# Performance work log

Hardware: AMD Instinct MI355X
Metric: run time of the kernel (lower is better)

## Reference

```python
import jax, jax.numpy as jnp
import numpy as np

B, S = 4, 1024          # 4 prefill sequences of length 1024 (cu_seqlens equal-length)
D_MODEL = 2048
N_HEADS = 32
N_KV_HEADS = 8
HEAD_DIM = D_MODEL // N_HEADS          # 64
GROUPS = N_HEADS // N_KV_HEADS         # 4
ROPE_THETA = 10000.0
SCALE = HEAD_DIM ** -0.5


def setup_inputs() -> dict:
    key = jax.random.key(0)
    ks = jax.random.split(key, 6)
    T = B * S
    hidden_states = jax.random.normal(ks[0], (T, D_MODEL), jnp.float32)
    # rotary tables: positions restart per sequence (prefill)
    pos = jnp.tile(jnp.arange(S, dtype=jnp.float32), B)            # [T]
    inv_freq = 1.0 / (ROPE_THETA ** (jnp.arange(0, HEAD_DIM, 2, dtype=jnp.float32) / HEAD_DIM))
    freqs = pos[:, None] * inv_freq[None, :]                        # [T, HEAD_DIM/2]
    cos, sin = jnp.cos(freqs), jnp.sin(freqs)
    std = D_MODEL ** -0.5
    Wq = jax.random.normal(ks[1], (D_MODEL, N_HEADS * HEAD_DIM), jnp.float32) * std
    Wk = jax.random.normal(ks[2], (D_MODEL, N_KV_HEADS * HEAD_DIM), jnp.float32) * std
    Wv = jax.random.normal(ks[3], (D_MODEL, N_KV_HEADS * HEAD_DIM), jnp.float32) * std
    Wo = jax.random.normal(ks[4], (N_HEADS * HEAD_DIM, D_MODEL), jnp.float32) * std
    return {"hidden_states": hidden_states, "cos": cos, "sin": sin,
            "Wq": Wq, "Wk": Wk, "Wv": Wv, "Wo": Wo}


def _rope(x, cos, sin):
    # NeoX-style rotary: x [T, H, D], cos/sin [T, D/2]
    half = x.shape[-1] // 2
    x1, x2 = x[..., :half], x[..., half:]
    c, s = cos[:, None, :], sin[:, None, :]
    return jnp.concatenate([x1 * c - x2 * s, x2 * c + x1 * s], axis=-1)


def reference(hidden_states, cos, sin, Wq, Wk, Wv, Wo):
    T = hidden_states.shape[0]
    q = (hidden_states @ Wq).reshape(T, N_HEADS, HEAD_DIM)
    k = (hidden_states @ Wk).reshape(T, N_KV_HEADS, HEAD_DIM)
    v = (hidden_states @ Wv).reshape(T, N_KV_HEADS, HEAD_DIM)
    q = _rope(q, cos, sin)
    k = _rope(k, cos, sin)
    # equal-length varlen prefill -> [B, S, H, D]
    q = q.reshape(B, S, N_HEADS, HEAD_DIM)
    k = jnp.repeat(k.reshape(B, S, N_KV_HEADS, HEAD_DIM), GROUPS, axis=2)  # GQA expand
    v = jnp.repeat(v.reshape(B, S, N_KV_HEADS, HEAD_DIM), GROUPS, axis=2)
    scores = jnp.einsum("bqhd,bkhd->bhqk", q, k) * SCALE
    causal = jnp.tril(jnp.ones((S, S), dtype=bool))
    scores = jnp.where(causal[None, None], scores, jnp.finfo(scores.dtype).min)
    probs = jax.nn.softmax(scores, axis=-1)
    attn = jnp.einsum("bhqk,bkhd->bqhd", probs, v).reshape(T, N_HEADS * HEAD_DIM)
    return attn @ Wo
```

## Files before the change

kernel.cpp:

```cpp
#include <hip/hip_runtime.h>
#include <type_traits>


typedef __bf16 bf16x8 __attribute__((ext_vector_type(8)));
typedef __bf16 bf16x4 __attribute__((ext_vector_type(4)));
typedef float f32x4 __attribute__((ext_vector_type(4)));
typedef unsigned short u16;
typedef unsigned int u32;

#define DEVI __device__ __forceinline__

DEVI u16 f2bf(float f) {
  u32 u = __builtin_bit_cast(u32, f);
  u += 0x7FFF + ((u >> 16) & 1);
  return (u16)(u >> 16);
}

DEVI void ld16_lds(const void* g, void* l) {
  __builtin_amdgcn_global_load_lds((const __attribute__((address_space(1))) u32*)g,
                                   (__attribute__((address_space(3))) u32*)l, 16, 0, 0);
}

template <int N> DEVI void waitvm() {
  if constexpr (N == 0) asm volatile("s_waitcnt vmcnt(0)" ::: "memory");
  else if constexpr (N == 6) asm volatile("s_waitcnt vmcnt(6)" ::: "memory");
  else if constexpr (N == 7) asm volatile("s_waitcnt vmcnt(7)" ::: "memory");
  else static_assert(N == 0, "unsupported vmcnt");
}
DEVI void lgkm0() {
  asm volatile("s_waitcnt lgkmcnt(0)" ::: "memory");
  __builtin_amdgcn_sched_barrier(0);
}
DEVI void barrier() { __builtin_amdgcn_s_barrier(); }

__global__ __launch_bounds__(256) void convert_f32_bf16(const float* __restrict__ src,
                                                        u16* __restrict__ dst, int n4) {
  int i = blockIdx.x * 256 + threadIdx.x;
  if (i >= n4) return;
  float4 v = ((const float4*)src)[i];
  ushort4 o;
  o.x = f2bf(v.x); o.y = f2bf(v.y); o.z = f2bf(v.z); o.w = f2bf(v.w);
  ((ushort4*)dst)[i] = o;
}

__global__ __launch_bounds__(256) void trans_f32_bf16(const float* __restrict__ src,
                                                      u16* __restrict__ dst, int R, int C,
                                                      float scale) {
  __shared__ float tile[32][33];
  int c0 = blockIdx.x * 32, r0 = blockIdx.y * 32;
  int tx = threadIdx.x & 31, ty = threadIdx.x >> 5;
#pragma unroll
  for (int i = 0; i < 32; i += 8)
    tile[ty + i][tx] = src[(size_t)(r0 + ty + i) * C + (c0 + tx)];
  __syncthreads();
#pragma unroll
  for (int i = 0; i < 32; i += 8)
    dst[(size_t)(c0 + ty + i) * R + (r0 + tx)] = f2bf(tile[tx][ty + i] * scale);
}

template <typename OutT, int BN>
__global__ __launch_bounds__(512, 2) void gemm8(const u16* __restrict__ A,
                                                const u16* __restrict__ BT,
                                                OutT* __restrict__ C, int M, int N, int K) {
  constexpr int WN = BN / 64;
  constexpr int NH0 = (WN + 1) / 2;
  constexpr int NH1 = WN - NH0;
  constexpr int VMW = 4 + WN;
  __shared__ u16 As[2][256 * 64];
  __shared__ u16 Bs[2][BN * 64];
  const int tid = threadIdx.x;
  const int lane = tid & 63, wave = tid >> 6;
  const int quad = lane >> 4, l16 = lane & 15;

  const int nwg = gridDim.x * gridDim.y;
  const int bid = blockIdx.y * gridDim.x + blockIdx.x;
  const int swz = (bid & 7) * (nwg >> 3) + (bid >> 3);
  const int m0 = (swz / gridDim.x) * 256, n0 = (swz % gridDim.x) * BN;
  const int wr = wave >> 2, wc = wave & 3;

  f32x4 acc[8][WN] = {};

  auto stageA = [&](int t, int h) {
    u16* D = &As[t & 1][h * 8192];
    const u16* G = A + (size_t)m0 * K + t * 64;
#pragma unroll
    for (int i = 0; i < 2; ++i) {
      int id = i * 512 + tid;
      int row = h * 128 + (id >> 3), ch = id & 7;
      ld16_lds(G + (size_t)row * K + (ch ^ (row & 7)) * 8, D + id * 8);
    }
  };
  auto stageB = [&](int t, int u) {
    u16* D = &Bs[t & 1][u * 4096];
    const u16* G = BT + (size_t)n0 * K + t * 64;
    int row = u * 64 + (tid >> 3), ch = tid & 7;
    ld16_lds(G + (size_t)row * K + (ch ^ (row & 7)) * 8, D + tid * 8);
  };
  auto stageBall = [&](int t) {
#pragma unroll
    for (int u = 0; u < WN; ++u) stageB(t, u);
  };

  bf16x8 af[4][2], bv0[NH0][2], bv1[NH1][2];
  auto ldA = [&](int msub, int d) {
#pragma unroll
    for (int i = 0; i < 4; ++i)
#pragma unroll
      for (int ks = 0; ks < 2; ++ks) {
        int r = wr * 128 + msub * 64 + i * 16 + l16;
        af[i][ks] = *(const bf16x8*)&As[d][r * 64 + (((ks * 4 + quad) ^ (r & 7)) * 8)];
      }
  };
  auto ldB0 = [&](int d) {
#pragma unroll
    for (int j = 0; j < NH0; ++j)
#pragma unroll
      for (int ks = 0; ks < 2; ++ks) {
        int rb = wc * (16 * WN) + j * 16 + l16;
        bv0[j][ks] = *(const bf16x8*)&Bs[d][rb * 64 + (((ks * 4 + quad) ^ (rb & 7)) * 8)];
      }
  };
  auto ldB1 = [&](int d) {
#pragma unroll
    for (int j = 0; j < NH1; ++j)
#pragma unroll
      for (int ks = 0; ks < 2; ++ks) {
        int rb = wc * (16 * WN) + (NH0 + j) * 16 + l16;
        bv1[j][ks] = *(const bf16x8*)&Bs[d][rb * 64 + (((ks * 4 + quad) ^ (rb & 7)) * 8)];
      }
  };
  auto mm0 = [&](int mo) {
    __builtin_amdgcn_s_setprio(1);
#pragma unroll
    for (int i = 0; i < 4; ++i)
#pragma unroll
      for (int j = 0; j < NH0; ++j)
#pragma unroll
        for (int ks = 0; ks < 2; ++ks)
          acc[mo + i][j] =
              __builtin_amdgcn_mfma_f32_16x16x32_bf16(af[i][ks], bv0[j][ks], acc[mo + i][j], 0, 0, 0);
    __builtin_amdgcn_s_setprio(0);
  };
  auto mm1 = [&](int mo) {
    __builtin_amdgcn_s_setprio(1);
#pragma unroll
    for (int i = 0; i < 4; ++i)
#pragma unroll
      for (int j = 0; j < NH1; ++j)
#pragma unroll
        for (int ks = 0; ks < 2; ++ks)
          acc[mo + i][NH0 + j] =
              __builtin_amdgcn_mfma_f32_16x16x32_bf16(af[i][ks], bv1[j][ks], acc[mo + i][NH0 + j], 0, 0, 0);
    __builtin_amdgcn_s_setprio(0);
  };

  const int NT = K / 64;

  stageA(0, 0); stageA(0, 1); stageBall(0);
  stageA(1, 0); stageA(1, 1); stageBall(1);
  waitvm<VMW>();
  barrier();

#pragma unroll 1
  for (int T = 0; T < NT; T += 2) {
    const bool pf = (T + 2 < NT);
    ldA(0, 0); ldB0(0);
    barrier(); lgkm0();
    mm0(0);
    barrier();

    ldB1(0);
    barrier(); lgkm0();
    mm1(0);
    barrier();

    ldA(1, 0);
    if (pf) stageBall(T + 2);
    barrier(); lgkm0();
    mm1(4);
    barrier();

    if (pf) {
      stageA(T + 2, 0); stageA(T + 2, 1);
      waitvm<VMW>();
    } else {
      waitvm<0>();
    }
    barrier();
    __builtin_amdgcn_sched_barrier(0);
    mm0(4);
    barrier();

    ldA(0, 1); ldB0(1);
    barrier(); lgkm0();
    mm0(0);
    barrier();

    ldB1(1);
    barrier(); lgkm0();
    mm1(0);
    barrier();

    ldA(1, 1);
    if (pf) stageBall(T + 3);
    barrier(); lgkm0();
    mm1(4);
    barrier();

    if (pf) {
      stageA(T + 3, 0); stageA(T + 3, 1);
      waitvm<VMW>();
      barrier();
      __builtin_amdgcn_sched_barrier(0);
      mm0(4);
      barrier();
    } else {
      mm0(4);
    }
  }

#pragma unroll
  for (int i = 0; i < 8; i++) {
    int row = m0 + wr * 128 + i * 16 + quad * 4;
#pragma unroll
    for (int j = 0; j < WN; j++) {
      int col = n0 + wc * (16 * WN) + j * 16 + l16;
#pragma unroll
      for (int r = 0; r < 4; r++) {
        size_t off = (size_t)(row + r) * N + col;
        if constexpr (sizeof(OutT) == 2) C[off] = f2bf(acc[i][j][r]);
        else C[off] = acc[i][j][r];
      }
    }
  }
}

__global__ __launch_bounds__(256) void rope_vkt(u16* __restrict__ qkv,
                                                u16* __restrict__ vkt,
                                                const float* __restrict__ cs,
                                                const float* __restrict__ sn) {
  const int kt = blockIdx.x, h = blockIdx.y, b = blockIdx.z;
  const int tid = threadIdx.x;
  const size_t tok0 = (size_t)b * 1024 + (size_t)kt * 128;

  {
    const int r = tid >> 1, hf = tid & 1;
    const size_t t = tok0 + r;
    const float* cr = cs + t * 32;
    const float* sr = sn + t * 32;
    u16* qrow = qkv + t * 3072 + h * 64;
    u16* krow = qkv + t * 3072 + 2048 + h * 64;
#pragma unroll
    for (int gg = 0; gg < 2; ++gg) {
      const int g = hf * 2 + gg;
      float cv[8], sv[8];
#pragma unroll
      for (int e = 0; e < 8; ++e) { cv[e] = cr[g * 8 + e]; sv[e] = sr[g * 8 + e]; }
      {
        bf16x8 a = *(bf16x8*)&qrow[g * 8];
        bf16x8 b2 = *(bf16x8*)&qrow[g * 8 + 32];
#pragma unroll
        for (int e = 0; e < 8; ++e) {
          float x1 = (float)a[e], x2 = (float)b2[e];
          a[e] = (__bf16)(x1 * cv[e] - x2 * sv[e]);
          b2[e] = (__bf16)(x2 * cv[e] + x1 * sv[e]);
        }
        *(bf16x8*)&qrow[g * 8] = a;
        *(bf16x8*)&qrow[g * 8 + 32] = b2;
      }
      if (h < 8) {
        bf16x8 a = *(bf16x8*)&krow[g * 8];
        bf16x8 b2 = *(bf16x8*)&krow[g * 8 + 32];
#pragma unroll
        for (int e = 0; e < 8; ++e) {
          float x1 = (float)a[e], x2 = (float)b2[e];
          a[e] = (__bf16)(x1 * cv[e] - x2 * sv[e]);
          b2[e] = (__bf16)(x2 * cv[e] + x1 * sv[e]);
        }
        *(bf16x8*)&krow[g * 8] = a;
        *(bf16x8*)&krow[g * 8 + 32] = b2;
      }
    }
  }
  if (h >= 8) return;

  __shared__ u16 Vn[128 * 64];
  const u16* src = qkv + tok0 * 3072 + 2560 + h * 64;
  {
    int tok = tid >> 1, hf = tid & 1;
    const uint4* s4 = (const uint4*)(src + (size_t)tok * 3072 + hf * 32);
    uint4* d4 = (uint4*)&Vn[tok * 64 + hf * 32];
#pragma unroll
    for (int j = 0; j < 4; j++) d4[j] = s4[j];
  }
  __syncthreads();
  u16* img = vkt + ((((size_t)b * 8 + h) * 8 + kt) << 13);
#pragma unroll
  for (int i = 0; i < 4; i++) {
    int c = tid * 4 + i;
    int dd = c >> 4, chsw = c & 15;
    int ch = chsw ^ (dd & 15);
    u16 tmp[8];
#pragma unroll
    for (int p = 0; p < 8; p++) {
      int col = ch * 8 + p;
      int g = col >> 5, kl = col & 31;
      int kph = ((kl >> 2) & 1) * 16 + ((kl >> 4) & 1) * 8 + ((kl >> 3) & 1) * 4 + (kl & 3);
      tmp[p] = Vn[(g * 32 + kph) * 64 + dd];
    }
    *(uint4*)&img[c * 8] = *(const uint4*)tmp;
  }
}

__global__ __launch_bounds__(256, 2) void flash_attn(const u16* __restrict__ qkv,
                                                     const u16* __restrict__ vkt,
                                                     u16* __restrict__ attn) {
  __shared__ u16 Ks[2][128 * 64];
  __shared__ u16 VT[2][64 * 128];

  const int tid = threadIdx.x;
  const int lane = tid & 63, wave = tid >> 6;
  const int quad = lane >> 4, l16 = lane & 15;
  const int qtA = blockIdx.x, qtB = 7 - blockIdx.x;
  const int h = blockIdx.y, b = blockIdx.z, kvh = h >> 2;
  const size_t tokBase = (size_t)b * 1024;
  const int qcol = h * 64, kcol = 2048 + kvh * 64;
  const int srow = tid >> 3, spc = tid & 7, ssc = spc ^ (srow & 7);

  auto stageK = [&](const u16* gbase, u16* L) {
#pragma unroll
    for (int i = 0; i < 4; i++)
      ld16_lds(gbase + (size_t)(srow + i * 32) * 3072 + ssc * 8, &L[tid * 8 + i * 2048]);
  };
  const u16* vimg = vkt + (((size_t)b * 8 + kvh) << 16);
  auto stageV = [&](int kt, u16* L) {
    const u16* g = vimg + ((size_t)kt << 13);
#pragma unroll
    for (int i = 0; i < 4; i++)
      ld16_lds(g + i * 2048 + tid * 8, &L[tid * 8 + i * 2048]);
  };

  stageK(qkv + (tokBase + qtA * 128) * 3072 + qcol, Ks[0]);
  stageK(qkv + (tokBase + qtB * 128) * 3072 + qcol, Ks[1]);
  __syncthreads();
  bf16x8 qfA[2][2], qfB[2][2];
#pragma unroll
  for (int nq = 0; nq < 2; nq++) {
    int qrow = wave * 32 + nq * 16 + l16;
#pragma unroll
    for (int ks = 0; ks < 2; ks++) {
      int c = (ks * 4 + quad) ^ (qrow & 7);
      qfA[nq][ks] = *(const bf16x8*)&Ks[0][qrow * 64 + c * 8];
      qfB[nq][ks] = *(const bf16x8*)&Ks[1][qrow * 64 + c * 8];
    }
  }
  __syncthreads();

  float lA[2] = {0.f, 0.f}, lB[2] = {0.f, 0.f};
  f32x4 oA[4][2] = {}, oB[4][2] = {};

  auto proc = [&](const bf16x8 (&kf)[2][2], const bf16x8 (&va)[4], const bf16x8 (&qf)[2][2],
                  f32x4 (&o)[4][2], float (&lacc)[2], bool msk, int c) {
    f32x4 s[2][2] = {};
    __builtin_amdgcn_s_setprio(1);
#pragma unroll
    for (int mkl = 0; mkl < 2; mkl++)
#pragma unroll
      for (int ks = 0; ks < 2; ks++) {
        s[0][mkl] = __builtin_amdgcn_mfma_f32_16x16x32_bf16(kf[mkl][ks], qf[0][ks], s[0][mkl], 0, 0, 0);
        s[1][mkl] = __builtin_amdgcn_mfma_f32_16x16x32_bf16(kf[mkl][ks], qf[1][ks], s[1][mkl], 0, 0, 0);
      }
    __builtin_amdgcn_s_setprio(0);
    if (msk) {
#pragma unroll
      for (int nq = 0; nq < 2; nq++) {
        int q = wave * 32 + nq * 16 + l16;
#pragma unroll
        for (int mkl = 0; mkl < 2; mkl++)
#pragma unroll
          for (int r = 0; r < 4; r++)
            if ((c * 2 + mkl) * 16 + quad * 4 + r > q) s[nq][mkl][r] = -3e38f;
      }
    }
    bf16x8 pf[2];
#pragma unroll
    for (int nq = 0; nq < 2; nq++) {
      float a0 = 0.f;
#pragma unroll
      for (int mkl = 0; mkl < 2; mkl++)
#pragma unroll
        for (int r = 0; r < 4; r++) {
          float p = __builtin_amdgcn_exp2f(s[nq][mkl][r]);
          s[nq][mkl][r] = p;
          a0 += p;
        }
      lacc[nq] += a0;
      pf[nq][0] = (__bf16)s[nq][0][0]; pf[nq][1] = (__bf16)s[nq][0][1];
      pf[nq][2] = (__bf16)s[nq][0][2]; pf[nq][3] = (__bf16)s[nq][0][3];
      pf[nq][4] = (__bf16)s[nq][1][0]; pf[nq][5] = (__bf16)s[nq][1][1];
      pf[nq][6] = (__bf16)s[nq][1][2]; pf[nq][7] = (__bf16)s[nq][1][3];
    }
    __builtin_amdgcn_s_setprio(1);
#pragma unroll
    for (int md = 0; md < 4; md++) {
      o[md][0] = __builtin_amdgcn_mfma_f32_16x16x32_bf16(va[md], pf[0], o[md][0], 0, 0, 0);
      o[md][1] = __builtin_amdgcn_mfma_f32_16x16x32_bf16(va[md], pf[1], o[md][1], 0, 0, 0);
    }
    __builtin_amdgcn_s_setprio(0);
  };

  stageK(qkv + tokBase * 3072 + kcol, Ks[0]);
  stageV(0, VT[0]);

  for (int kt = 0; kt <= qtB; kt++) {
    const int cur = kt & 1;
    __syncthreads();
    if (kt < qtB) {
      stageK(qkv + (tokBase + (kt + 1) * 128) * 3072 + kcol, Ks[1 - cur]);
      stageV(kt + 1, VT[1 - cur]);
    }
    const bool doA = (kt <= qtA), mA = (kt == qtA), mB = (kt == qtB);
    const u16* K = Ks[cur];
    const u16* V = VT[cur];
#pragma unroll
    for (int c = 0; c < 4; c++) {
      bf16x8 kf[2][2];
#pragma unroll
      for (int mkl = 0; mkl < 2; mkl++) {
        int krow = (c * 2 + mkl) * 16 + l16;
#pragma unroll
        for (int ks = 0; ks < 2; ks++)
          kf[mkl][ks] = *(const bf16x8*)&K[krow * 64 + ((ks * 4 + quad) ^ (krow & 7)) * 8];
      }
      bf16x8 va[4];
#pragma unroll
      for (int md = 0; md < 4; md++) {
        int dd = md * 16 + l16;
        va[md] = *(const bf16x8*)&V[dd * 128 + ((c * 4 + quad) ^ l16) * 8];
      }
      proc(kf, va, qfB, oB, lB, mB, c);
      if (doA) proc(kf, va, qfA, oA, lA, mA, c);
    }
  }

  auto epilogue = [&](const f32x4 (&o)[4][2], const float (&lacc)[2], int qt_tile) {
#pragma unroll
    for (int nq = 0; nq < 2; nq++) {
      float l = lacc[nq];
      l += __shfl_xor(l, 16);
      l += __shfl_xor(l, 32);
      float inv = 1.0f / l;
      int t = qt_tile * 128 + wave * 32 + nq * 16 + l16;
      size_t rowOff = (tokBase + t) * 2048 + qcol;
#pragma unroll
      for (int md = 0; md < 4; md++) {
        bf16x4 w;
        w[0] = (__bf16)(o[md][nq][0] * inv);
        w[1] = (__bf16)(o[md][nq][1] * inv);
        w[2] = (__bf16)(o[md][nq][2] * inv);
        w[3] = (__bf16)(o[md][nq][3] * inv);
        *(bf16x4*)&attn[rowOff + md * 16 + quad * 4] = w;
      }
    }
  };
  epilogue(oB, lB, qtB);
  epilogue(oA, lA, qtA);
}

extern "C" void kernel_launch(void* const* d_in, const int* in_sizes, int n_in,
                              void* d_out, int out_size, void* d_ws, size_t ws_size,
                              hipStream_t stream) {
  const float* hs = (const float*)d_in[0];
  const float* cs = (const float*)d_in[1];
  const float* sn = (const float*)d_in[2];
  const float* Wq = (const float*)d_in[3];
  const float* Wk = (const float*)d_in[4];
  const float* Wv = (const float*)d_in[5];
  const float* Wo = (const float*)d_in[6];
  float* out = (float*)d_out;

  char* ws = (char*)d_ws;
  u16* hsB   = (u16*)(ws);
  u16* vkt   = (u16*)(ws);
  u16* wqkvT = (u16*)(ws + 16777216);
  u16* woT   = (u16*)(ws + 29360128);
  u16* qkv   = (u16*)(ws + 37748736);
  u16* attnB = (u16*)(ws + 62914560);

  const float QSCALE = 0.18033688011112042f;

  convert_f32_bf16<<<8192, 256, 0, stream>>>(hs, hsB, 4096 * 2048 / 4);
  trans_f32_bf16<<<dim3(64, 64), 256, 0, stream>>>(Wq, wqkvT, 2048, 2048, QSCALE);
  trans_f32_bf16<<<dim3(16, 64), 256, 0, stream>>>(Wk, wqkvT + (size_t)2048 * 2048, 2048, 512, 1.0f);
  trans_f32_bf16<<<dim3(16, 64), 256, 0, stream>>>(Wv, wqkvT + (size_t)2560 * 2048, 2048, 512, 1.0f);
  trans_f32_bf16<<<dim3(64, 64), 256, 0, stream>>>(Wo, woT, 2048, 2048, 1.0f);

  gemm8<u16, 192><<<dim3(16, 16), 512, 0, stream>>>(hsB, wqkvT, qkv, 4096, 3072, 2048);
  rope_vkt<<<dim3(8, 32, 4), 256, 0, stream>>>(qkv, vkt, cs, sn);
  flash_attn<<<dim3(4, 32, 4), 256, 0, stream>>>(qkv, vkt, attnB);
  gemm8<float, 128><<<dim3(16, 16), 512, 0, stream>>>(attnB, woT, out, 4096, 2048, 2048);
}
```

Before: 272.7 us.

## Fuse prep conversion kernels and retile GEMMs to 128-row, 4-wave blocks

New measurement: 253.7 us. 7.0% less time.

```diff
diff --git a/kernel.cpp b/kernel.cpp
--- a/kernel.cpp
+++ b/kernel.cpp
@@ -25,6 +25,8 @@
   if constexpr (N == 0) asm volatile("s_waitcnt vmcnt(0)" ::: "memory");
   else if constexpr (N == 6) asm volatile("s_waitcnt vmcnt(6)" ::: "memory");
   else if constexpr (N == 7) asm volatile("s_waitcnt vmcnt(7)" ::: "memory");
+  else if constexpr (N == 8) asm volatile("s_waitcnt vmcnt(8)" ::: "memory");
+  else if constexpr (N == 10) asm volatile("s_waitcnt vmcnt(10)" ::: "memory");
   else static_assert(N == 0, "unsupported vmcnt");
 }
 DEVI void lgkm0() {
@@ -33,21 +35,28 @@
 }
 DEVI void barrier() { __builtin_amdgcn_s_barrier(); }
 
-__global__ __launch_bounds__(256) void convert_f32_bf16(const float* __restrict__ src,
-                                                        u16* __restrict__ dst, int n4) {
-  int i = blockIdx.x * 256 + threadIdx.x;
-  if (i >= n4) return;
-  float4 v = ((const float4*)src)[i];
-  ushort4 o;
-  o.x = f2bf(v.x); o.y = f2bf(v.y); o.z = f2bf(v.z); o.w = f2bf(v.w);
-  ((ushort4*)dst)[i] = o;
-}
-
-__global__ __launch_bounds__(256) void trans_f32_bf16(const float* __restrict__ src,
-                                                      u16* __restrict__ dst, int R, int C,
-                                                      float scale) {
+__global__ __launch_bounds__(256) void prep(const float* __restrict__ hs, u16* __restrict__ hsB,
+                                            const float* __restrict__ Wq, const float* __restrict__ Wk,
+                                            const float* __restrict__ Wv, const float* __restrict__ Wo,
+                                            u16* __restrict__ wqkvT, u16* __restrict__ woT,
+                                            float qscale) {
+  int b = blockIdx.x;
+  if (b < 8192) {
+    int i = b * 256 + threadIdx.x;
+    float4 v = ((const float4*)hs)[i];
+    ushort4 o;
+    o.x = f2bf(v.x); o.y = f2bf(v.y); o.z = f2bf(v.z); o.w = f2bf(v.w);
+    ((ushort4*)hsB)[i] = o;
+    return;
+  }
+  b -= 8192;
+  const float* src; u16* dst; int R, C, bx, by; float sc = 1.0f;
+  if (b < 4096)      { src = Wq; dst = wqkvT;                         R = 2048; C = 2048; bx = b & 63; by = b >> 6; sc = qscale; }
+  else if (b < 5120) { b -= 4096; src = Wk; dst = wqkvT + (size_t)2048 * 2048; R = 2048; C = 512; bx = b & 15; by = b >> 4; }
+  else if (b < 6144) { b -= 5120; src = Wv; dst = wqkvT + (size_t)2560 * 2048; R = 2048; C = 512; bx = b & 15; by = b >> 4; }
+  else               { b -= 6144; src = Wo; dst = woT;                R = 2048; C = 2048; bx = b & 63; by = b >> 6; }
   __shared__ float tile[32][33];
-  int c0 = blockIdx.x * 32, r0 = blockIdx.y * 32;
+  int c0 = bx * 32, r0 = by * 32;
   int tx = threadIdx.x & 31, ty = threadIdx.x >> 5;
 #pragma unroll
   for (int i = 0; i < 32; i += 8)
@@ -55,18 +64,21 @@
   __syncthreads();
 #pragma unroll
   for (int i = 0; i < 32; i += 8)
-    dst[(size_t)(c0 + ty + i) * R + (r0 + tx)] = f2bf(tile[tx][ty + i] * scale);
+    dst[(size_t)(c0 + ty + i) * R + (r0 + tx)] = f2bf(tile[tx][ty + i] * sc);
 }
 
 template <typename OutT, int BN>
-__global__ __launch_bounds__(512, 2) void gemm8(const u16* __restrict__ A,
+__global__ __launch_bounds__(256, 2) void gemm2(const u16* __restrict__ A,
                                                 const u16* __restrict__ BT,
                                                 OutT* __restrict__ C, int M, int N, int K) {
-  constexpr int WN = BN / 64;
-  constexpr int NH0 = (WN + 1) / 2;
-  constexpr int NH1 = WN - NH0;
-  constexpr int VMW = 4 + WN;
-  __shared__ u16 As[2][256 * 64];
+  constexpr int NF = BN / 32;
+  constexpr int NH = NF / 2;
+  constexpr int HW = BN / 2;
+  constexpr int SW = HW / 2;
+  constexpr int LB0 = BN / 64;
+  constexpr int VMW = 4 + 2 * LB0;
+  constexpr int VMP = 4 + LB0;
+  __shared__ u16 As[2][128 * 64];
   __shared__ u16 Bs[2][BN * 64];
   const int tid = threadIdx.x;
   const int lane = tid & 63, wave = tid >> 6;
@@ -75,158 +87,96 @@
   const int nwg = gridDim.x * gridDim.y;
   const int bid = blockIdx.y * gridDim.x + blockIdx.x;
   const int swz = (bid & 7) * (nwg >> 3) + (bid >> 3);
-  const int m0 = (swz / gridDim.x) * 256, n0 = (swz % gridDim.x) * BN;
-  const int wr = wave >> 2, wc = wave & 3;
-
-  f32x4 acc[8][WN] = {};
-
-  auto stageA = [&](int t, int h) {
-    u16* D = &As[t & 1][h * 8192];
+  const int m0 = (swz / gridDim.x) * 128, n0 = (swz % gridDim.x) * BN;
+  const int wr = wave >> 1, wc = wave & 1;
+
+  f32x4 acc[4][NF] = {};
+
+  auto stA = [&](int t) {
+    u16* D = &As[t & 1][0];
     const u16* G = A + (size_t)m0 * K + t * 64;
 #pragma unroll
-    for (int i = 0; i < 2; ++i) {
-      int id = i * 512 + tid;
-      int row = h * 128 + (id >> 3), ch = id & 7;
+    for (int i = 0; i < 4; ++i) {
+      int id = i * 256 + tid, row = id >> 3, ch = id & 7;
       ld16_lds(G + (size_t)row * K + (ch ^ (row & 7)) * 8, D + id * 8);
     }
   };
-  auto stageB = [&](int t, int u) {
-    u16* D = &Bs[t & 1][u * 4096];
-    const u16* G = BT + (size_t)n0 * K + t * 64;
-    int row = u * 64 + (tid >> 3), ch = tid & 7;
-    ld16_lds(G + (size_t)row * K + (ch ^ (row & 7)) * 8, D + tid * 8);
-  };
-  auto stageBall = [&](int t) {
-#pragma unroll
-    for (int u = 0; u < WN; ++u) stageB(t, u);
-  };
-
-  bf16x8 af[4][2], bv0[NH0][2], bv1[NH1][2];
-  auto ldA = [&](int msub, int d) {
+  auto stB = [&](int t, int h) {
+    u16* D = &Bs[t & 1][h * HW * 64];
+    const u16* G = BT + (size_t)(n0 + h * HW) * K + t * 64;
+#pragma unroll
+    for (int i = 0; i < LB0; ++i) {
+      int id = i * 256 + tid, row = id >> 3, ch = id & 7;
+      ld16_lds(G + (size_t)row * K + (ch ^ (row & 7)) * 8, D + id * 8);
+    }
+  };
+
+  bf16x8 af[4][2], bv0[NH][2], bv1[NH][2];
+  auto ldA = [&](int d) {
 #pragma unroll
     for (int i = 0; i < 4; ++i)
 #pragma unroll
       for (int ks = 0; ks < 2; ++ks) {
-        int r = wr * 128 + msub * 64 + i * 16 + l16;
+        int r = wr * 64 + i * 16 + l16;
         af[i][ks] = *(const bf16x8*)&As[d][r * 64 + (((ks * 4 + quad) ^ (r & 7)) * 8)];
       }
   };
-  auto ldB0 = [&](int d) {
-#pragma unroll
-    for (int j = 0; j < NH0; ++j)
+  auto ldB = [&](bf16x8 (&bv)[NH][2], int half, int d) {
+#pragma unroll
+    for (int j = 0; j < NH; ++j)
 #pragma unroll
       for (int ks = 0; ks < 2; ++ks) {
-        int rb = wc * (16 * WN) + j * 16 + l16;
-        bv0[j][ks] = *(const bf16x8*)&Bs[d][rb * 64 + (((ks * 4 + quad) ^ (rb & 7)) * 8)];
-      }
-  };
-  auto ldB1 = [&](int d) {
-#pragma unroll
-    for (int j = 0; j < NH1; ++j)
-#pragma unroll
-      for (int ks = 0; ks < 2; ++ks) {
-        int rb = wc * (16 * WN) + (NH0 + j) * 16 + l16;
-        bv1[j][ks] = *(const bf16x8*)&Bs[d][rb * 64 + (((ks * 4 + quad) ^ (rb & 7)) * 8)];
-      }
-  };
-  auto mm0 = [&](int mo) {
+        int rb = half * HW + wc * SW + j * 16 + l16;
+        bv[j][ks] = *(const bf16x8*)&Bs[d][rb * 64 + (((ks * 4 + quad) ^ (rb & 7)) * 8)];
+      }
+  };
+  auto mm = [&](bf16x8 (&bv)[NH][2], int jo) {
     __builtin_amdgcn_s_setprio(1);
 #pragma unroll
     for (int i = 0; i < 4; ++i)
 #pragma unroll
-      for (int j = 0; j < NH0; ++j)
+      for (int j = 0; j < NH; ++j)
 #pragma unroll
         for (int ks = 0; ks < 2; ++ks)
-          acc[mo + i][j] =
-              __builtin_amdgcn_mfma_f32_16x16x32_bf16(af[i][ks], bv0[j][ks], acc[mo + i][j], 0, 0, 0);
+          acc[i][jo + j] =
+              __builtin_amdgcn_mfma_f32_16x16x32_bf16(af[i][ks], bv[j][ks], acc[i][jo + j], 0, 0, 0);
     __builtin_amdgcn_s_setprio(0);
   };
-  auto mm1 = [&](int mo) {
-    __builtin_amdgcn_s_setprio(1);
-#pragma unroll
-    for (int i = 0; i < 4; ++i)
-#pragma unroll
-      for (int j = 0; j < NH1; ++j)
-#pragma unroll
-        for (int ks = 0; ks < 2; ++ks)
-          acc[mo + i][NH0 + j] =
-              __builtin_amdgcn_mfma_f32_16x16x32_bf16(af[i][ks], bv1[j][ks], acc[mo + i][NH0 + j], 0, 0, 0);
-    __builtin_amdgcn_s_setprio(0);
-  };
 
   const int NT = K / 64;
 
-  stageA(0, 0); stageA(0, 1); stageBall(0);
-  stageA(1, 0); stageA(1, 1); stageBall(1);
-  waitvm<VMW>();
+  stA(0); stB(0, 0); stB(0, 1);
+  stA(1); stB(1, 0);
+  waitvm<VMP>();
   barrier();
 
-#pragma unroll 1
-  for (int T = 0; T < NT; T += 2) {
-    const bool pf = (T + 2 < NT);
-    ldA(0, 0); ldB0(0);
+#pragma unroll 2
+  for (int t = 0; t < NT; ++t) {
+    const int buf = t & 1;
+    const bool deep = (t + 2 < NT);
+    ldA(buf); ldB(bv0, 0, buf);
+    if (t + 1 < NT) stB(t + 1, 1);
     barrier(); lgkm0();
-    mm0(0);
+    mm(bv0, 0);
+    if (deep) waitvm<VMW>(); else waitvm<0>();
     barrier();
-
-    ldB1(0);
+    ldB(bv1, 1, buf);
+    if (deep) { stA(t + 2); stB(t + 2, 0); }
     barrier(); lgkm0();
-    mm1(0);
+    mm(bv1, NH);
+    if (deep) waitvm<VMW>(); else waitvm<0>();
     barrier();
-
-    ldA(1, 0);
-    if (pf) stageBall(T + 2);
-    barrier(); lgkm0();
-    mm1(4);
-    barrier();
-
-    if (pf) {
-      stageA(T + 2, 0); stageA(T + 2, 1);
-      waitvm<VMW>();
-    } else {
-      waitvm<0>();
-    }
-    barrier();
-    __builtin_amdgcn_sched_barrier(0);
-    mm0(4);
-    barrier();
-
-    ldA(0, 1); ldB0(1);
-    barrier(); lgkm0();
-    mm0(0);
-    barrier();
-
-    ldB1(1);
-    barrier(); lgkm0();
-    mm1(0);
-    barrier();
-
-    ldA(1, 1);
-    if (pf) stageBall(T + 3);
-    barrier(); lgkm0();
-    mm1(4);
-    barrier();
-
-    if (pf) {
-      stageA(T + 3, 0); stageA(T + 3, 1);
-      waitvm<VMW>();
-      barrier();
-      __builtin_amdgcn_sched_barrier(0);
-      mm0(4);
-      barrier();
-    } else {
-      mm0(4);
-    }
-  }
-
-#pragma unroll
-  for (int i = 0; i < 8; i++) {
-    int row = m0 + wr * 128 + i * 16 + quad * 4;
-#pragma unroll
-    for (int j = 0; j < WN; j++) {
-      int col = n0 + wc * (16 * WN) + j * 16 + l16;
-#pragma unroll
-      for (int r = 0; r < 4; r++) {
+  }
+
+#pragma unroll
+  for (int i = 0; i < 4; ++i) {
+    int row = m0 + wr * 64 + i * 16 + quad * 4;
+#pragma unroll
+    for (int j = 0; j < NF; ++j) {
+      int half = j / NH, jj = j % NH;
+      int col = n0 + half * HW + wc * SW + jj * 16 + l16;
+#pragma unroll
+      for (int r = 0; r < 4; ++r) {
         size_t off = (size_t)(row + r) * N + col;
         if constexpr (sizeof(OutT) == 2) C[off] = f2bf(acc[i][j][r]);
         else C[off] = acc[i][j][r];
@@ -489,14 +439,10 @@
 
   const float QSCALE = 0.18033688011112042f;
 
-  convert_f32_bf16<<<8192, 256, 0, stream>>>(hs, hsB, 4096 * 2048 / 4);
-  trans_f32_bf16<<<dim3(64, 64), 256, 0, stream>>>(Wq, wqkvT, 2048, 2048, QSCALE);
-  trans_f32_bf16<<<dim3(16, 64), 256, 0, stream>>>(Wk, wqkvT + (size_t)2048 * 2048, 2048, 512, 1.0f);
-  trans_f32_bf16<<<dim3(16, 64), 256, 0, stream>>>(Wv, wqkvT + (size_t)2560 * 2048, 2048, 512, 1.0f);
-  trans_f32_bf16<<<dim3(64, 64), 256, 0, stream>>>(Wo, woT, 2048, 2048, 1.0f);
-
-  gemm8<u16, 192><<<dim3(16, 16), 512, 0, stream>>>(hsB, wqkvT, qkv, 4096, 3072, 2048);
+  prep<<<18432, 256, 0, stream>>>(hs, hsB, Wq, Wk, Wv, Wo, wqkvT, woT, QSCALE);
+
+  gemm2<u16, 192><<<dim3(16, 32), 256, 0, stream>>>(hsB, wqkvT, qkv, 4096, 3072, 2048);
   rope_vkt<<<dim3(8, 32, 4), 256, 0, stream>>>(qkv, vkt, cs, sn);
   flash_attn<<<dim3(4, 32, 4), 256, 0, stream>>>(qkv, vkt, attnB);
-  gemm8<float, 128><<<dim3(16, 16), 512, 0, stream>>>(attnB, woT, out, 4096, 2048, 2048);
-}
+  gemm2<float, 128><<<dim3(16, 32), 256, 0, stream>>>(attnB, woT, out, 4096, 2048, 2048);
+}
```
